# Kernel tuning notes

Measured on AMD Instinct MI355X. Metric: run time of the kernel, lower is better.

## Reference

```python
import math
import jax, jax.numpy as jnp
import numpy as np

GROUPS = 32
EPS = 1e-5


def group_norm(x, gamma, beta):
    # x: (b, c, h, w); normalize per-group over (c/g, h, w)
    b, c, h, w = x.shape
    xg = x.reshape(b, GROUPS, c // GROUPS, h, w)
    mu = xg.mean(axis=(2, 3, 4), keepdims=True)
    var = xg.var(axis=(2, 3, 4), keepdims=True)
    xn = ((xg - mu) * jax.lax.rsqrt(var + EPS)).reshape(b, c, h, w)
    return xn * gamma[None, :, None, None] + beta[None, :, None, None]


def conv1x1(x, w, bias):
    # x: (b, c, h, w), w: (o, c) -> (b, o, h, w)
    return jnp.einsum('bchw,oc->bohw', x, w) + bias[None, :, None, None]


def setup_inputs() -> dict:
    key = jax.random.key(0)
    ks = jax.random.split(key, 7)
    b, c, h, w = 8, 512, 32, 32
    s = 1.0 / math.sqrt(c)
    return {
        'x': jax.random.normal(ks[0], (b, c, h, w), dtype=jnp.float32),
        'gn_w': jnp.ones((c,), dtype=jnp.float32),
        'gn_b': jnp.zeros((c,), dtype=jnp.float32),
        'qkv_w': jax.random.normal(ks[1], (3 * c, c), dtype=jnp.float32) * s,
        'qkv_b': jnp.zeros((3 * c,), dtype=jnp.float32),
        'proj_w': jax.random.normal(ks[2], (c, c), dtype=jnp.float32) * s,
        'proj_b': jnp.zeros((c,), dtype=jnp.float32),
        'num_heads': 8,
    }


def reference(x, gn_w, gn_b, qkv_w, qkv_b, proj_w, proj_b, num_heads):
    b, c, h, w = x.shape
    hds = num_heads
    d = c // hds
    x_ = group_norm(x, gn_w, gn_b)
    qkv = conv1x1(x_, qkv_w, qkv_b)  # (b, 3c, h, w)
    q, k, v = jnp.split(qkv, 3, axis=1)
    # (b, hds, d, hw)
    q = q.reshape(b, hds, d, h * w)
    k = k.reshape(b, hds, d, h * w)
    v = v.reshape(b, hds, d, h * w)
    # scores: (b, hds, hw, hw) = q^T k / sqrt(d)
    scores = jnp.einsum('bhdq,bhdk->bhqk', q, k) / math.sqrt(d)
    attn = jax.nn.softmax(scores, axis=-1)
    # out = (attn @ v^T)^T -> (b, hds, d, hw)
    out = jnp.einsum('bhqk,bhdk->bhdq', attn, v)
    out = out.reshape(b, c, h, w)
    return x + conv1x1(out, proj_w, proj_b)
```

## Files before the change

kernel.cpp:

```cpp
#include <hip/hip_runtime.h>


typedef __attribute__((ext_vector_type(8))) short short8v;
typedef __attribute__((ext_vector_type(4))) short short4v;
typedef __attribute__((ext_vector_type(4))) float f32x4;
typedef __attribute__((ext_vector_type(2))) unsigned uint2v;

constexpr int Bn = 8, Cn = 512, HWn = 1024, CGn = 16;

#if __has_builtin(__builtin_amdgcn_exp2f)
#define EXP2F(x) __builtin_amdgcn_exp2f(x)
#else
#define EXP2F(x) __exp2f(x)
#endif

static __device__ __forceinline__ short bf16_of(float f) {
  union { float f; unsigned u; } v{f};
  unsigned r = v.u + 0x7fffu + ((v.u >> 16) & 1u);
  return (short)(r >> 16);
}
static __device__ __forceinline__ unsigned bf16pk(float a, float b) {
  return (unsigned)(unsigned short)bf16_of(a) |
         ((unsigned)(unsigned short)bf16_of(b) << 16);
}

static __device__ __forceinline__ void gload16(const void* g, void* l) {
  __builtin_amdgcn_global_load_lds(
      (const __attribute__((address_space(1))) unsigned*)g,
      (__attribute__((address_space(3))) unsigned*)l, 16, 0, 0);
}

__global__ __launch_bounds__(256) void prep_k(const float* __restrict__ x,
                                              float* __restrict__ stats,
                                              const float* __restrict__ wq,
                                              const float* __restrict__ wp,
                                              short* __restrict__ oq,
                                              short* __restrict__ op) {
  if (blockIdx.x >= 256) {
    int i = (blockIdx.x - 256) * 256 + threadIdx.x;
    const float* src = wq;
    short* dst = oq;
    int idx = i;
    if (i >= 196608) { src = wp; dst = op; idx = i - 196608; }
    f32x4 v = ((const f32x4*)src)[idx];
    short4v o;
    o.x = bf16_of(v.x); o.y = bf16_of(v.y); o.z = bf16_of(v.z); o.w = bf16_of(v.w);
    *(short4v*)&dst[idx * 4] = o;
    return;
  }
  int bg = blockIdx.x;
  const f32x4* p = (const f32x4*)(x + (size_t)bg * (CGn * HWn));
  float s = 0.f, ss = 0.f;
  for (int i = threadIdx.x; i < CGn * HWn / 4; i += 256) {
    f32x4 v = p[i];
    s += v.x + v.y + v.z + v.w;
    ss += v.x * v.x + v.y * v.y + v.z * v.z + v.w * v.w;
  }
#pragma unroll
  for (int off = 32; off; off >>= 1) {
    s += __shfl_xor(s, off);
    ss += __shfl_xor(ss, off);
  }
  __shared__ float rs[4], rss[4];
  int lane = threadIdx.x & 63, w = threadIdx.x >> 6;
  if (lane == 0) { rs[w] = s; rss[w] = ss; }
  __syncthreads();
  if (threadIdx.x == 0) {
    float S = rs[0] + rs[1] + rs[2] + rs[3];
    float SS = rss[0] + rss[1] + rss[2] + rss[3];
    const float invn = 1.0f / (CGn * HWn);
    float mu = S * invn;
    float var = SS * invn - mu * mu;
    stats[bg] = mu;
    stats[256 + bg] = rsqrtf(var + 1e-5f);
  }
}

__global__ __launch_bounds__(256) void gn_apply_t_k(const float* __restrict__ x,
                                                    const float* __restrict__ stats,
                                                    const float* __restrict__ gw,
                                                    const float* __restrict__ gb,
                                                    short* __restrict__ xnT) {
  __shared__ __align__(16) short T[64][72];
  const int hw0 = blockIdx.x * 64, c0 = blockIdx.y * 64, b = blockIdx.z;
  const float* xb = x + ((size_t)b * Cn + c0) * HWn + hw0;
  const int t = threadIdx.x;
  const int cr = t >> 4, h4 = (t & 15) * 4;
#pragma unroll
  for (int i = 0; i < 4; i++) {
    int c = cr + 16 * i;
    int cg = c0 + c;
    int bg = b * 32 + (cg >> 4);
    float mu = stats[bg], rstd = stats[256 + bg];
    float ga = gw[cg] * rstd;
    float be = gb[cg] - mu * ga;
    f32x4 v = *(const f32x4*)&xb[(size_t)c * HWn + h4];
    T[h4 + 0][c] = bf16_of(fmaf(v.x, ga, be));
    T[h4 + 1][c] = bf16_of(fmaf(v.y, ga, be));
    T[h4 + 2][c] = bf16_of(fmaf(v.z, ga, be));
    T[h4 + 3][c] = bf16_of(fmaf(v.w, ga, be));
  }
  __syncthreads();
  short* dst = xnT + ((size_t)b * HWn + hw0) * Cn + c0;
  const int hr = t >> 3, c8 = (t & 7) * 8;
#pragma unroll
  for (int i = 0; i < 2; i++) {
    int r = hr + 32 * i;
    *(short8v*)&dst[(size_t)r * Cn + c8] = *(const short8v*)&T[r][c8];
  }
}

__device__ __forceinline__ short8v fragG(const short* buf, int row, int gk) {
  return *(const short8v*)&buf[row * 32 + ((gk ^ ((row >> 1) & 3)) << 3)];
}

template <int MODE>
__global__ __launch_bounds__(256, 2) void gemm_bf16_k(
    const short* __restrict__ A, const short* __restrict__ Bt,
    const float* __restrict__ bias, const float* __restrict__ resid,
    float* __restrict__ outF, short* __restrict__ oQ, short* __restrict__ oK,
    short* __restrict__ oV) {
  constexpr int MB = (MODE == 0) ? 12 : 4;
  const int bid = blockIdx.x;
  const int swz = (bid & 7) * (8 * MB) + (bid >> 3);
  const int bn = swz & 7;
  const int rest = swz >> 3;
  const int bm = rest % MB, b = rest / MB;
  const bool VBLK = (MODE == 0) && (bm >= 8);

  const short* Bb = Bt + (size_t)b * HWn * Cn;
  __shared__ __align__(16) short As[128 * 32];
  __shared__ __align__(16) short Bs[128 * 32];
  const int t = threadIdx.x, l = t & 63, w = t >> 6;
  const int wr = w >> 1, wc = w & 1;
  const int m0 = bm * 128, n0 = bn * 128;
  const f32x4 vzero = {0.f, 0.f, 0.f, 0.f};
  f32x4 acc[4][4];
#pragma unroll
  for (int i = 0; i < 4; i++)
#pragma unroll
    for (int j = 0; j < 4; j++) acc[i][j] = vzero;

  const int rA0 = w * 16 + (l >> 2);
  const int g0 = l & 3;

  for (int k0 = 0; k0 < 512; k0 += 32) {
#pragma unroll
    for (int it = 0; it < 2; it++) {
      int r = rA0 + it * 64;
      int gs = g0 ^ ((r >> 1) & 3);
      gload16(&A[(size_t)(m0 + r) * 512 + k0 + gs * 8], &As[it * 2048 + w * 512]);
      gload16(&Bb[(size_t)(n0 + r) * 512 + k0 + gs * 8], &Bs[it * 2048 + w * 512]);
    }
    __syncthreads();
    short8v af[4], bf[4];
#pragma unroll
    for (int i = 0; i < 4; i++) af[i] = fragG(As, wr * 64 + i * 16 + (l & 15), l >> 4);
#pragma unroll
    for (int j = 0; j < 4; j++) bf[j] = fragG(Bs, wc * 64 + j * 16 + (l & 15), l >> 4);
    if (VBLK) {
#pragma unroll
      for (int i = 0; i < 4; i++)
#pragma unroll
        for (int j = 0; j < 4; j++)
          acc[i][j] = __builtin_amdgcn_mfma_f32_16x16x32_bf16(bf[j], af[i], acc[i][j], 0, 0, 0);
    } else {
#pragma unroll
      for (int i = 0; i < 4; i++)
#pragma unroll
        for (int j = 0; j < 4; j++)
          acc[i][j] = __builtin_amdgcn_mfma_f32_16x16x32_bf16(af[i], bf[j], acc[i][j], 0, 0, 0);
    }
    __syncthreads();
  }

  if (MODE == 1) {
    float* outb = outF + (size_t)b * Cn * HWn;
    const float* rb = resid + (size_t)b * Cn * HWn;
#pragma unroll
    for (int i = 0; i < 4; i++) {
      f32x4 bv = *(const f32x4*)&bias[m0 + wr * 64 + i * 16 + (l >> 4) * 4];
#pragma unroll
      for (int r = 0; r < 4; r++) {
        int m = m0 + wr * 64 + i * 16 + (l >> 4) * 4 + r;
#pragma unroll
        for (int j = 0; j < 4; j++) {
          int n = n0 + wc * 64 + j * 16 + (l & 15);
          size_t idx = (size_t)m * HWn + n;
          outb[idx] = acc[i][j][r] + bv[r] + rb[idx];
        }
      }
    }
  } else if (!VBLK) {
    short* oBase = (m0 < 512) ? oQ : oK;
    const int mc = (m0 < 512 ? m0 : m0 - 512) + wr * 64;
#pragma unroll
    for (int i = 0; i < 4; i++) {
      int mi = mc + i * 16 + (l >> 4) * 4;
      f32x4 bv = *(const f32x4*)&bias[m0 + wr * 64 + i * 16 + (l >> 4) * 4];
#pragma unroll
      for (int j = 0; j < 4; j++) {
        int n = n0 + wc * 64 + j * 16 + (l & 15);
        uint2v pk = {bf16pk(acc[i][j][0] + bv[0], acc[i][j][1] + bv[1]),
                     bf16pk(acc[i][j][2] + bv[2], acc[i][j][3] + bv[3])};
        *(uint2v*)&oBase[((size_t)b * HWn + n) * 512 + mi] = pk;
      }
    }
  } else {
#pragma unroll
    for (int i = 0; i < 4; i++) {
      int m = m0 + wr * 64 + i * 16 + (l & 15);
      float bv = bias[m];
      short* vrow = oV + ((size_t)b * 512 + (m - 1024)) * HWn;
#pragma unroll
      for (int j = 0; j < 4; j++) {
        int n = n0 + wc * 64 + j * 16 + (l >> 4) * 4;
        uint2v pk = {bf16pk(acc[i][j][0] + bv, acc[i][j][1] + bv),
                     bf16pk(acc[i][j][2] + bv, acc[i][j][3] + bv)};
        *(uint2v*)&vrow[n] = pk;
      }
    }
  }
}

__device__ __forceinline__ short8v frag64(const short* buf, int row, int gk) {
  return *(const short8v*)&buf[row * 64 + ((gk ^ (row & 7)) << 3)];
}
__device__ __forceinline__ short8v frag128(const short* buf, int row, int gk) {
  return *(const short8v*)&buf[row * 128 + ((gk ^ (row & 7)) << 3)];
}

__global__ __launch_bounds__(512, 4) void attn_k(const short* __restrict__ qT,
                                                 const short* __restrict__ kT,
                                                 const short* __restrict__ vB,
                                                 short* __restrict__ aoT) {
  const int bid = blockIdx.x;
  const int swz = (bid & 7) * 64 + (bid >> 3);
  const int qt = swz & 7, head = (swz >> 3) & 7, b = swz >> 6;
  __shared__ __align__(16) short SM[33792];
  short* Ks = SM;
  short* Vs = SM + 8192;
  short* Ps = SM + 16384;
  const int t = threadIdx.x, l = t & 63, w = t >> 6;
  short* Psw = Ps + w * 2176;
  const f32x4 vzero = {0.f, 0.f, 0.f, 0.f};

  const short* ksrc = kT + (size_t)b * HWn * 512 + head * 64;
  const short* vsrc = vB + ((size_t)b * 512 + head * 64) * HWn;

  const short* qrow = qT +
      ((size_t)b * HWn + qt * 128 + 16 * w + (l & 15)) * 512 + head * 64 +
      (l >> 4) * 8;
  const short8v qf0 = *(const short8v*)&qrow[0];
  const short8v qf1 = *(const short8v*)&qrow[32];

  const int kkv0 = w * 8 + (l >> 3), kg = l & 7;
  const int vd0 = w * 4 + (l >> 4), vg = l & 15;

  f32x4 oa[4];
#pragma unroll
  for (int f = 0; f < 4; f++) oa[f] = vzero;
  float m_run = -1e30f, l_run = 0.f;
  constexpr float SC = 0.1803368801111f;

#pragma unroll 1
  for (int kt = 0; kt < 8; kt++) {
    __syncthreads();
#pragma unroll
    for (int it = 0; it < 2; it++) {
      int kv = kkv0 + it * 64;
      gload16(&ksrc[(size_t)(kt * 128 + kv) * 512 + (kg ^ (kv & 7)) * 8],
              &Ks[it * 4096 + w * 512]);
      int d = vd0 + it * 32;
      gload16(&vsrc[(size_t)d * HWn + kt * 128 + (vg ^ (d & 7)) * 8],
              &Vs[it * 4096 + w * 512]);
    }
    __syncthreads();

    f32x4 sa[8];
    __builtin_amdgcn_s_setprio(1);
#pragma unroll
    for (int f = 0; f < 8; f++) {
      short8v ka0 = frag64(Ks, 16 * f + (l & 15), l >> 4);
      short8v ka1 = frag64(Ks, 16 * f + (l & 15), (l >> 4) + 4);
      sa[f] = __builtin_amdgcn_mfma_f32_16x16x32_bf16(ka0, qf0, vzero, 0, 0, 0);
      sa[f] = __builtin_amdgcn_mfma_f32_16x16x32_bf16(ka1, qf1, sa[f], 0, 0, 0);
    }
    __builtin_amdgcn_s_setprio(0);

    float p[8][4];
    float mt = -1e30f;
#pragma unroll
    for (int f = 0; f < 8; f++)
#pragma unroll
      for (int r = 0; r < 4; r++) {
        float s = sa[f][r] * SC;
        p[f][r] = s;
        mt = fmaxf(mt, s);
      }
    mt = fmaxf(mt, __shfl_xor(mt, 16));
    mt = fmaxf(mt, __shfl_xor(mt, 32));
    if (__any(mt > m_run + 8.f)) {
      float mn = fmaxf(m_run, mt);
      float corr = EXP2F(m_run - mn);
      m_run = mn;
      l_run *= corr;
      float cr[4];
#pragma unroll
      for (int r = 0; r < 4; r++) cr[r] = __shfl(corr, 4 * (l >> 4) + r);
#pragma unroll
      for (int f = 0; f < 4; f++)
#pragma unroll
        for (int r = 0; r < 4; r++) oa[f][r] *= cr[r];
    }
    float ps = 0.f;
#pragma unroll
    for (int f = 0; f < 8; f++)
#pragma unroll
      for (int r = 0; r < 4; r++) {
        float e = EXP2F(p[f][r] - m_run);
        p[f][r] = e;
        ps += e;
      }
    ps += __shfl_xor(ps, 16);
    ps += __shfl_xor(ps, 32);
    l_run += ps;

#pragma unroll
    for (int f = 0; f < 8; f++) {
      int o = (l & 15) * 136 + 16 * f + 4 * (l >> 4);
      uint2v pk = {bf16pk(p[f][0], p[f][1]), bf16pk(p[f][2], p[f][3])};
      *(uint2v*)&Psw[o] = pk;
    }
    short8v pa[4];
#pragma unroll
    for (int c = 0; c < 4; c++)
      pa[c] = *(const short8v*)&Psw[(l & 15) * 136 + c * 32 + (l >> 4) * 8];
    __builtin_amdgcn_s_setprio(1);
#pragma unroll
    for (int fd = 0; fd < 4; fd++) {
      int row = 16 * fd + (l & 15);
#pragma unroll
      for (int c = 0; c < 4; c++) {
        short8v vb = frag128(Vs, row, c * 4 + (l >> 4));
        oa[fd] = __builtin_amdgcn_mfma_f32_16x16x32_bf16(pa[c], vb, oa[fd], 0, 0, 0);
      }
    }
    __builtin_amdgcn_s_setprio(0);
  }

  const float inv = 1.0f / l_run;
  float iv[4];
#pragma unroll
  for (int r = 0; r < 4; r++) iv[r] = __shfl(inv, 4 * (l >> 4) + r);
#pragma unroll
  for (int r = 0; r < 4; r++)
#pragma unroll
    for (int f = 0; f < 4; f++)
      Psw[(4 * (l >> 4) + r) * 136 + 16 * f + (l & 15)] =
          bf16_of(oa[f][r] * iv[r]);
  __syncthreads();
  short* dst = aoT + ((size_t)b * HWn + qt * 128) * 512 + head * 64;
#pragma unroll
  for (int it = 0; it < 2; it++) {
    int r = (t >> 3) + 64 * it;
    int c8 = (t & 7) * 8;
    *(short8v*)&dst[(size_t)r * 512 + c8] =
        *(const short8v*)&Ps[(r >> 4) * 2176 + (r & 15) * 136 + c8];
  }
}

extern "C" void kernel_launch(void* const* d_in, const int* in_sizes, int n_in,
                              void* d_out, int out_size, void* d_ws, size_t ws_size,
                              hipStream_t stream) {
  const float* x = (const float*)d_in[0];
  const float* gn_w = (const float*)d_in[1];
  const float* gn_b = (const float*)d_in[2];
  const float* qkv_w = (const float*)d_in[3];
  const float* qkv_b = (const float*)d_in[4];
  const float* proj_w = (const float*)d_in[5];
  const float* proj_b = (const float*)d_in[6];
  float* out = (float*)d_out;

  char* ws = (char*)d_ws;
  float* stats = (float*)ws;
  short* wqb = (short*)(ws + 4096);
  short* wpb = (short*)(ws + 4096 + 1572864);
  char* p = ws + 4096 + 1572864 + 524288;
  const size_t SB = (size_t)Bn * HWn * 512 * 2;
  short* xnT = (short*)p;
  short* qT = (short*)(p + SB);
  short* kT = (short*)(p + 2 * SB);
  short* vB = (short*)(p + 3 * SB);
  short* aoT = (short*)(p + 4 * SB);

  prep_k<<<1280, 256, 0, stream>>>(x, stats, qkv_w, proj_w, wqb, wpb);
  gn_apply_t_k<<<dim3(16, 8, 8), 256, 0, stream>>>(x, stats, gn_w, gn_b, xnT);
  gemm_bf16_k<0><<<768, 256, 0, stream>>>(wqb, xnT, qkv_b, nullptr, nullptr, qT, kT, vB);
  attn_k<<<512, 512, 0, stream>>>(qT, kT, vB, aoT);
  gemm_bf16_k<1><<<256, 256, 0, stream>>>(wpb, aoT, proj_b, x, out, nullptr,
                                          nullptr, nullptr);
}
```

Before: 89.13 us.

## Deepen GEMM K-tile to 64 and prefetch attention K/V tiles via registers

The GEMM kernel now stages 64-wide K slices with an 8-way XOR swizzle, halving the number of loop iterations and barriers per tile at the cost of twice the shared memory. The attention kernel preloads the first K/V tile, then prefetches the next tile into registers while computing on the current one, and writes it to LDS after compute. This hides global load latency behind the MFMA and softmax work. Softmax scaling is folded into a single fma inside exp2, with the rescale threshold expressed in raw score units. The register prefetch raises register pressure and keeps two barriers per iteration.

```diff
diff --git a/kernel.cpp b/kernel.cpp
--- a/kernel.cpp
+++ b/kernel.cpp
@@ -110,8 +110,11 @@
   }
 }
 
-__device__ __forceinline__ short8v fragG(const short* buf, int row, int gk) {
-  return *(const short8v*)&buf[row * 32 + ((gk ^ ((row >> 1) & 3)) << 3)];
+__device__ __forceinline__ short8v frag64(const short* buf, int row, int gk) {
+  return *(const short8v*)&buf[row * 64 + ((gk ^ (row & 7)) << 3)];
+}
+__device__ __forceinline__ short8v frag128(const short* buf, int row, int gk) {
+  return *(const short8v*)&buf[row * 128 + ((gk ^ (row & 7)) << 3)];
 }
 
 template <int MODE>
@@ -129,8 +132,8 @@
   const bool VBLK = (MODE == 0) && (bm >= 8);
 
   const short* Bb = Bt + (size_t)b * HWn * Cn;
-  __shared__ __align__(16) short As[128 * 32];
-  __shared__ __align__(16) short Bs[128 * 32];
+  __shared__ __align__(16) short As[128 * 64];
+  __shared__ __align__(16) short Bs[128 * 64];
   const int t = threadIdx.x, l = t & 63, w = t >> 6;
   const int wr = w >> 1, wc = w & 1;
   const int m0 = bm * 128, n0 = bn * 128;
@@ -141,35 +144,40 @@
 #pragma unroll
     for (int j = 0; j < 4; j++) acc[i][j] = vzero;
 
-  const int rA0 = w * 16 + (l >> 2);
-  const int g0 = l & 3;
-
-  for (int k0 = 0; k0 < 512; k0 += 32) {
-#pragma unroll
-    for (int it = 0; it < 2; it++) {
-      int r = rA0 + it * 64;
-      int gs = g0 ^ ((r >> 1) & 3);
+  const int sr0 = t >> 3;
+  const int sg = t & 7;
+
+  for (int k0 = 0; k0 < 512; k0 += 64) {
+#pragma unroll
+    for (int it = 0; it < 4; it++) {
+      int r = it * 32 + sr0;
+      int gs = sg ^ (r & 7);
       gload16(&A[(size_t)(m0 + r) * 512 + k0 + gs * 8], &As[it * 2048 + w * 512]);
       gload16(&Bb[(size_t)(n0 + r) * 512 + k0 + gs * 8], &Bs[it * 2048 + w * 512]);
     }
     __syncthreads();
-    short8v af[4], bf[4];
-#pragma unroll
-    for (int i = 0; i < 4; i++) af[i] = fragG(As, wr * 64 + i * 16 + (l & 15), l >> 4);
-#pragma unroll
-    for (int j = 0; j < 4; j++) bf[j] = fragG(Bs, wc * 64 + j * 16 + (l & 15), l >> 4);
-    if (VBLK) {
+#pragma unroll
+    for (int kk = 0; kk < 2; kk++) {
+      short8v af[4], bf[4];
 #pragma unroll
       for (int i = 0; i < 4; i++)
-#pragma unroll
-        for (int j = 0; j < 4; j++)
-          acc[i][j] = __builtin_amdgcn_mfma_f32_16x16x32_bf16(bf[j], af[i], acc[i][j], 0, 0, 0);
-    } else {
-#pragma unroll
-      for (int i = 0; i < 4; i++)
-#pragma unroll
-        for (int j = 0; j < 4; j++)
-          acc[i][j] = __builtin_amdgcn_mfma_f32_16x16x32_bf16(af[i], bf[j], acc[i][j], 0, 0, 0);
+        af[i] = frag64(As, wr * 64 + i * 16 + (l & 15), kk * 4 + (l >> 4));
+#pragma unroll
+      for (int j = 0; j < 4; j++)
+        bf[j] = frag64(Bs, wc * 64 + j * 16 + (l & 15), kk * 4 + (l >> 4));
+      if (VBLK) {
+#pragma unroll
+        for (int i = 0; i < 4; i++)
+#pragma unroll
+          for (int j = 0; j < 4; j++)
+            acc[i][j] = __builtin_amdgcn_mfma_f32_16x16x32_bf16(bf[j], af[i], acc[i][j], 0, 0, 0);
+      } else {
+#pragma unroll
+        for (int i = 0; i < 4; i++)
+#pragma unroll
+          for (int j = 0; j < 4; j++)
+            acc[i][j] = __builtin_amdgcn_mfma_f32_16x16x32_bf16(af[i], bf[j], acc[i][j], 0, 0, 0);
+      }
     }
     __syncthreads();
   }
@@ -221,13 +229,6 @@
       }
     }
   }
-}
-
-__device__ __forceinline__ short8v frag64(const short* buf, int row, int gk) {
-  return *(const short8v*)&buf[row * 64 + ((gk ^ (row & 7)) << 3)];
-}
-__device__ __forceinline__ short8v frag128(const short* buf, int row, int gk) {
-  return *(const short8v*)&buf[row * 128 + ((gk ^ (row & 7)) << 3)];
 }
 
 __global__ __launch_bounds__(512, 4) void attn_k(const short* __restrict__ qT,
@@ -257,25 +258,37 @@
   const int kkv0 = w * 8 + (l >> 3), kg = l & 7;
   const int vd0 = w * 4 + (l >> 4), vg = l & 15;
 
+#pragma unroll
+  for (int it = 0; it < 2; it++) {
+    int kv = kkv0 + it * 64;
+    gload16(&ksrc[(size_t)kv * 512 + (kg ^ (kv & 7)) * 8], &Ks[it * 4096 + w * 512]);
+    int d = vd0 + it * 32;
+    gload16(&vsrc[(size_t)d * HWn + (vg ^ (d & 7)) * 8], &Vs[it * 4096 + w * 512]);
+  }
+  __syncthreads();
+
   f32x4 oa[4];
 #pragma unroll
   for (int f = 0; f < 4; f++) oa[f] = vzero;
   float m_run = -1e30f, l_run = 0.f;
   constexpr float SC = 0.1803368801111f;
+  constexpr float THRraw = 44.3614195558f;
 
 #pragma unroll 1
   for (int kt = 0; kt < 8; kt++) {
-    __syncthreads();
-#pragma unroll
-    for (int it = 0; it < 2; it++) {
-      int kv = kkv0 + it * 64;
-      gload16(&ksrc[(size_t)(kt * 128 + kv) * 512 + (kg ^ (kv & 7)) * 8],
-              &Ks[it * 4096 + w * 512]);
-      int d = vd0 + it * 32;
-      gload16(&vsrc[(size_t)d * HWn + kt * 128 + (vg ^ (d & 7)) * 8],
-              &Vs[it * 4096 + w * 512]);
-    }
-    __syncthreads();
+    short8v kreg[2], vreg[2];
+    if (kt < 7) {
+      const int kt1 = kt + 1;
+#pragma unroll
+      for (int it = 0; it < 2; it++) {
+        int kv = kkv0 + it * 64;
+        kreg[it] = *(const short8v*)&ksrc[(size_t)(kt1 * 128 + kv) * 512 +
+                                          (kg ^ (kv & 7)) * 8];
+        int d = vd0 + it * 32;
+        vreg[it] = *(const short8v*)&vsrc[(size_t)d * HWn + kt1 * 128 +
+                                          (vg ^ (d & 7)) * 8];
+      }
+    }
 
     f32x4 sa[8];
     __builtin_amdgcn_s_setprio(1);
@@ -288,21 +301,16 @@
     }
     __builtin_amdgcn_s_setprio(0);
 
-    float p[8][4];
-    float mt = -1e30f;
+    float mt = -3e38f;
 #pragma unroll
     for (int f = 0; f < 8; f++)
 #pragma unroll
-      for (int r = 0; r < 4; r++) {
-        float s = sa[f][r] * SC;
-        p[f][r] = s;
-        mt = fmaxf(mt, s);
-      }
+      for (int r = 0; r < 4; r++) mt = fmaxf(mt, sa[f][r]);
     mt = fmaxf(mt, __shfl_xor(mt, 16));
     mt = fmaxf(mt, __shfl_xor(mt, 32));
-    if (__any(mt > m_run + 8.f)) {
+    if (__any(mt > m_run + THRraw)) {
       float mn = fmaxf(m_run, mt);
-      float corr = EXP2F(m_run - mn);
+      float corr = EXP2F((m_run - mn) * SC);
       m_run = mn;
       l_run *= corr;
       float cr[4];
@@ -313,13 +321,14 @@
 #pragma unroll
         for (int r = 0; r < 4; r++) oa[f][r] *= cr[r];
     }
+    const float mneg = -m_run * SC;
     float ps = 0.f;
 #pragma unroll
     for (int f = 0; f < 8; f++)
 #pragma unroll
       for (int r = 0; r < 4; r++) {
-        float e = EXP2F(p[f][r] - m_run);
-        p[f][r] = e;
+        float e = EXP2F(fmaf(sa[f][r], SC, mneg));
+        sa[f][r] = e;
         ps += e;
       }
     ps += __shfl_xor(ps, 16);
@@ -329,7 +338,7 @@
 #pragma unroll
     for (int f = 0; f < 8; f++) {
       int o = (l & 15) * 136 + 16 * f + 4 * (l >> 4);
-      uint2v pk = {bf16pk(p[f][0], p[f][1]), bf16pk(p[f][2], p[f][3])};
+      uint2v pk = {bf16pk(sa[f][0], sa[f][1]), bf16pk(sa[f][2], sa[f][3])};
       *(uint2v*)&Psw[o] = pk;
     }
     short8v pa[4];
@@ -347,6 +356,16 @@
       }
     }
     __builtin_amdgcn_s_setprio(0);
+
+    if (kt < 7) {
+      __syncthreads();
+#pragma unroll
+      for (int it = 0; it < 2; it++) {
+        *(short8v*)&Ks[it * 4096 + w * 512 + l * 8] = kreg[it];
+        *(short8v*)&Vs[it * 4096 + w * 512 + l * 8] = vreg[it];
+      }
+      __syncthreads();
+    }
   }
 
   const float inv = 1.0f / l_run;
```

Result: faster. 85.32 us (-4.3%).
